# Performance work log

Measured on AMD Instinct MI355X. Metric: run time of the kernel, lower is better.

Reference implementation:

```python
import jax, jax.numpy as jnp
import numpy as np

B, S, K, H = 8192, 512, 8, 512  # batch, size_half, n_segments, hidden
EPS = 1e-6


def setup_inputs() -> dict:
    key = jax.random.key(0)
    k0, k1, k2, k3 = jax.random.split(key, 4)
    x_input = jax.random.uniform(k0, (B, 2 * S), dtype=jnp.float32)  # in [0,1)
    log_density = jax.random.normal(k1, (B, 1), dtype=jnp.float32)
    W1 = jax.random.normal(k2, (S, H), dtype=jnp.float32) / np.sqrt(S).astype(np.float32)
    b1 = jnp.zeros((H,), jnp.float32)
    W2 = jax.random.normal(k3, (H, S * (2 * K + 1)), dtype=jnp.float32) / np.sqrt(H).astype(np.float32)
    b2 = jnp.zeros((S * (2 * K + 1),), jnp.float32)
    return {"x_input": x_input, "log_density": log_density,
            "W1": W1, "b1": b1, "W2": W2, "b2": b2}


def reference(x_input, log_density, W1, b1, W2, b2):
    # even_sites=True: passive half a = first S cols, transformed half b = last S
    x_a = x_input[:, :S]
    x_b = x_input[:, S:]

    # NeuralNetwork: Linear -> tanh -> Linear -> tanh (final_activation == activation)
    hid = jnp.tanh((x_a - 0.5) @ W1 + b1)
    net = jnp.tanh(hid @ W2 + b2).reshape(-1, S, 2 * K + 1)  # [B,S,2K+1]
    h_raw, w_raw = net[..., :K + 1], net[..., K + 1:]

    w_norm = jax.nn.softmax(w_raw, axis=2)                       # [B,S,K]
    eh = jnp.exp(h_raw)                                          # [B,S,K+1]
    h_norm = eh / jnp.sum(0.5 * w_norm * (eh[..., :-1] + eh[..., 1:]),
                          axis=2, keepdims=True)

    b = x_a.shape[0]
    x_knots = jnp.concatenate(
        [jnp.full((b, S, 1), -EPS, x_a.dtype), jnp.cumsum(w_norm, axis=2)], axis=2)  # [B,S,K+1]
    pdf_area = 0.5 * w_norm * (h_norm[..., :-1] + h_norm[..., 1:])
    phi_knots = jnp.concatenate(
        [jnp.zeros((b, S, 1), x_a.dtype), jnp.cumsum(pdf_area, axis=2)], axis=2)     # [B,S,K+1]

    # searchsorted(left) - 1 == (# knots strictly below x) - 1
    k_ind = jnp.clip(jnp.sum(x_knots < x_b[..., None], axis=2) - 1, 0, K - 1)[..., None]

    w_k = jnp.take_along_axis(w_norm, k_ind, axis=2)
    h_k = jnp.take_along_axis(h_norm, k_ind, axis=2)
    h_kp1 = jnp.take_along_axis(h_norm, k_ind + 1, axis=2)
    x_km1 = jnp.take_along_axis(x_knots, k_ind, axis=2)
    phi_km1 = jnp.take_along_axis(phi_knots, k_ind, axis=2)

    alpha = (x_b[..., None] - x_km1) / w_k
    phi_b = (phi_km1 + alpha * h_k * w_k
             + 0.5 * alpha ** 2 * (h_kp1 - h_k) * w_k)[..., 0]    # [B,S]

    phi_out = jnp.concatenate([x_a, phi_b], axis=1)               # [B,2S]
    new_log_density = log_density - jnp.sum(
        jnp.log(h_k + alpha * (h_kp1 - h_k)), axis=1)             # [B,1]
    return phi_out, new_log_density
```

## Files before the change

### kernel.cpp

```cpp
#include <hip/hip_runtime.h>
#include <stdint.h>
#include <math.h>

#define BROWS 8192
#define SDIM  512
#define HDIM  512
#define NCOL  8704
#define EPSK  1e-6f
#define LOG2E  1.442695041f
#define TWOL2E 2.885390082f
#define LN2    0.6931471806f

typedef __attribute__((ext_vector_type(8))) short bf16x8;
typedef __attribute__((ext_vector_type(4))) short bf16x4;
typedef __attribute__((ext_vector_type(4))) float f32x4;

__device__ __forceinline__ unsigned short f2bf(float f) {
    unsigned u = __float_as_uint(f);
    u += 0x7fffu + ((u >> 16) & 1u);
    return (unsigned short)(u >> 16);
}
__device__ __forceinline__ unsigned short f2bf_fast(float f) {
    return (unsigned short)((__float_as_uint(f) + 0x8000u) >> 16);
}
__device__ __forceinline__ float bf2f(unsigned short s) {
    return __uint_as_float(((unsigned)s) << 16);
}
#define EXP2F(x) __builtin_amdgcn_exp2f(x)
#define LOG2F(x) __builtin_amdgcn_logf(x)
#define RCPF(x)  __builtin_amdgcn_rcpf(x)

__device__ __forceinline__ float ftanh(float x) {
    float t = fminf(fmaxf(TWOL2E * x, -43.f), 43.f);
    float e = EXP2F(t);
    return (e - 1.f) * RCPF(e + 1.f);
}
__device__ __forceinline__ float ftanh_l2e(float acc, float bias2L) {
    float t = fminf(fmaxf(fmaf(acc, TWOL2E, bias2L), -43.f), 43.f);
    float e = EXP2F(t);
    return fmaf(e, LOG2E, -LOG2E) * RCPF(e + 1.f);
}

#define GLD16(g, l)                                                         \
    __builtin_amdgcn_global_load_lds(                                       \
        (const __attribute__((address_space(1))) void*)(g),                 \
        (__attribute__((address_space(3))) void*)(l), 16, 0, 0)

__global__ __launch_bounds__(256) void prep_k(
    const float* __restrict__ W2, unsigned short* __restrict__ W2p,
    const float* __restrict__ W1, unsigned short* __restrict__ W1T,
    const float* __restrict__ logd, float* __restrict__ out)
{
    __shared__ float tile[32 * 33];
    const int t = threadIdx.x;
    if (blockIdx.x < 544) {
        const int ct = blockIdx.x;
        const int colbase = ct * 16;
        const int colblk = ct / 17;
        const int chunk  = ct - colblk * 17;
        const int k32 = t >> 3;
        const int c2  = (t & 7) * 2;
        const int r   = t >> 4;
        const int e2  = (t & 15) * 2;
        for (int kk = 0; kk < 16; ++kk) {
            float2 v = *(const float2*)&W2[(size_t)(kk * 32 + k32) * NCOL + colbase + c2];
            __syncthreads();
            tile[k32 * 17 + c2 + 0] = v.x;
            tile[k32 * 17 + c2 + 1] = v.y;
            __syncthreads();
            const size_t off = (((size_t)colblk * 16 + kk) * 17 + chunk) * 512;
            ushort2 o;
            o.x = f2bf(tile[(e2 + 0) * 17 + r]);
            o.y = f2bf(tile[(e2 + 1) * 17 + r]);
            *(ushort2*)&W2p[off + (size_t)r * 32 + e2] = o;
        }
    } else if (blockIdx.x < 800) {
        const int bt = blockIdx.x - 544;
        const int cb = (bt & 15) * 32;
        const int rb = (bt >> 4) * 32;
        const int ty = t >> 3, tx = (t & 7) * 4;
        float4 v = *(const float4*)&W1[(size_t)(rb + ty) * HDIM + cb + tx];
        tile[ty * 33 + tx + 0] = v.x;
        tile[ty * 33 + tx + 1] = v.y;
        tile[ty * 33 + tx + 2] = v.z;
        tile[ty * 33 + tx + 3] = v.w;
        __syncthreads();
        const int oy = t >> 3, ox = (t & 7) * 4;
        bf16x4 o;
        o[0] = (short)f2bf(tile[(ox + 0) * 33 + oy]);
        o[1] = (short)f2bf(tile[(ox + 1) * 33 + oy]);
        o[2] = (short)f2bf(tile[(ox + 2) * 33 + oy]);
        o[3] = (short)f2bf(tile[(ox + 3) * 33 + oy]);
        *(bf16x4*)&W1T[(size_t)(cb + oy) * SDIM + rb + ox] = o;
    } else {
        const int b = (blockIdx.x - 800) * 256 + t;
        out[(size_t)BROWS * (2 * SDIM) + b] = logd[b];
    }
}

__global__ __launch_bounds__(256) void gemm1_mfma(
    const float* __restrict__ x,
    const unsigned short* __restrict__ W1T,
    const float* __restrict__ b1,
    unsigned short* __restrict__ hid,
    float* __restrict__ out)
{
    __shared__ short As[64 * 32];
    __shared__ short Bs[128 * 32];
    const int bm   = blockIdx.y * 64;
    const int bn   = blockIdx.x * 128;
    const int tid  = threadIdx.x;
    const int lane = tid & 63;
    const int wave = tid >> 6;
    const int ln15 = lane & 15;
    const int quad = lane >> 4;
    const int wm   = (wave >> 1) * 32;
    const int wn   = (wave & 1) * 64;
    const int arow = tid >> 2, aseg = tid & 3;
    const int brow = lane >> 2, bsub = lane & 3;

    f32x4 acc[2][4];
#pragma unroll
    for (int i = 0; i < 2; i++)
#pragma unroll
        for (int j = 0; j < 4; j++) acc[i][j] = (f32x4){0.f, 0.f, 0.f, 0.f};

    for (int k0 = 0; k0 < SDIM; k0 += 32) {
        const float4* xq = (const float4*)&x[(size_t)(bm + arow) * (2 * SDIM) + k0 + aseg * 8];
        float4 f0 = xq[0], f1 = xq[1];
        if (blockIdx.x == 0) {
            float* op = &out[(size_t)(bm + arow) * (2 * SDIM) + k0 + aseg * 8];
            *(float4*)op = f0;
            *(float4*)(op + 4) = f1;
        }
        __syncthreads();
#pragma unroll
        for (int c = 0; c < 2; c++) {
            const int chunk = wave * 2 + c;
            GLD16(&W1T[(size_t)(bn + chunk * 16 + brow) * SDIM + k0 + bsub * 8],
                  &Bs[chunk * 512]);
        }
        bf16x8 v0;
        v0[0] = (short)f2bf_fast(f0.x - 0.5f); v0[1] = (short)f2bf_fast(f0.y - 0.5f);
        v0[2] = (short)f2bf_fast(f0.z - 0.5f); v0[3] = (short)f2bf_fast(f0.w - 0.5f);
        v0[4] = (short)f2bf_fast(f1.x - 0.5f); v0[5] = (short)f2bf_fast(f1.y - 0.5f);
        v0[6] = (short)f2bf_fast(f1.z - 0.5f); v0[7] = (short)f2bf_fast(f1.w - 0.5f);
        *(bf16x8*)&As[arow * 32 + aseg * 8] = v0;
        __syncthreads();

        bf16x8 af[2], bfr[4];
#pragma unroll
        for (int i = 0; i < 2; i++)
            af[i] = *(const bf16x8*)&As[(wm + i * 16 + ln15) * 32 + quad * 8];
#pragma unroll
        for (int j = 0; j < 4; j++)
            bfr[j] = *(const bf16x8*)&Bs[(wn + j * 16 + ln15) * 32 + quad * 8];
#pragma unroll
        for (int i = 0; i < 2; i++)
#pragma unroll
            for (int j = 0; j < 4; j++)
                acc[i][j] = __builtin_amdgcn_mfma_f32_16x16x32_bf16(af[i], bfr[j], acc[i][j], 0, 0, 0);
    }

#pragma unroll
    for (int j = 0; j < 4; j++) {
        const int col = bn + wn + j * 16 + ln15;
        const float bias = b1[col];
#pragma unroll
        for (int i = 0; i < 2; i++) {
#pragma unroll
            for (int r = 0; r < 4; r++) {
                const int row = bm + wm + i * 16 + quad * 4 + r;
                hid[(size_t)row * HDIM + col] = f2bf(ftanh(acc[i][j][r] + bias));
            }
        }
    }
}

__global__ __launch_bounds__(256, 3) void gemm2_spline_mfma(
    const unsigned short* __restrict__ hid,
    const unsigned short* __restrict__ W2p,
    const float* __restrict__ b2,
    const float* __restrict__ x,
    float* __restrict__ out)
{
    __shared__ short smem[64 * 392];
    short* As = smem;
    short* Bs = smem + 2048;

    const int bm   = blockIdx.y * 64;
    const int tid  = threadIdx.x;
    const int lane = tid & 63;
    const int wave = tid >> 6;
    const int ln15 = lane & 15;
    const int quad = lane >> 4;
    const int brow = lane >> 2, bsub = lane & 3;
    const int jstart = wave * 4;
    const int jcount = (wave == 3) ? 5 : 4;
    const int bcol = blockIdx.x * 272;

    f32x4 acc[4][5];
#pragma unroll
    for (int i = 0; i < 4; i++)
#pragma unroll
        for (int j = 0; j < 5; j++) acc[i][j] = (f32x4){0.f, 0.f, 0.f, 0.f};

    const unsigned short* bbase =
        W2p + ((size_t)blockIdx.x * 16) * 17 * 512 + (size_t)lane * 8;

    for (int k0 = 0; k0 < HDIM; k0 += 32) {
        const unsigned short* bk = bbase + (size_t)(k0 >> 5) * (17 * 512);
        __syncthreads();
        GLD16(&hid[(size_t)(bm + wave * 16 + brow) * HDIM + k0 + bsub * 8],
              &As[wave * 512]);
        for (int c = 0; c < jcount; ++c) {
            const int chunk = jstart + c;
            GLD16(bk + (size_t)chunk * 512, &Bs[chunk * 512]);
        }
        __syncthreads();

        bf16x8 af[4];
#pragma unroll
        for (int i = 0; i < 4; i++)
            af[i] = *(const bf16x8*)&As[(i * 16 + ln15) * 32 + quad * 8];

#define KSTEP(JC)                                                               \
        _Pragma("unroll") for (int j = 0; j < (JC); ++j) {                      \
            bf16x8 bfr = *(const bf16x8*)&Bs[((jstart + j) * 16 + ln15) * 32 + quad * 8]; \
            _Pragma("unroll") for (int i = 0; i < 4; ++i)                       \
                acc[i][j] = __builtin_amdgcn_mfma_f32_16x16x32_bf16(af[i], bfr, acc[i][j], 0, 0, 0); \
        }
        if (wave == 3) { KSTEP(5) } else { KSTEP(4) }
#undef KSTEP
    }

    __syncthreads();
#define EPI1(JC)                                                                \
    _Pragma("unroll") for (int j = 0; j < (JC); ++j) {                          \
        const int col_l = (jstart + j) * 16 + ln15;                             \
        const int spc   = (col_l * 241) >> 12;         \
        const int cc    = col_l - spc * 17;                                     \
        const int basej = spc * 24 + cc;                                        \
        const float bias2L = b2[bcol + col_l] * TWOL2E;                         \
        _Pragma("unroll") for (int i = 0; i < 4; ++i)                           \
            _Pragma("unroll") for (int r = 0; r < 4; ++r) {                     \
                const int row_l = i * 16 + quad * 4 + r;                        \
                smem[row_l * 392 + basej] =                                     \
                    (short)f2bf_fast(ftanh_l2e(acc[i][j][r], bias2L));          \
            }                                                                   \
    }
    if (wave == 3) { EPI1(5) } else { EPI1(4) }
#undef EPI1
    __syncthreads();

    const int sp = tid & 15;
    const int r0 = tid >> 4;
    const int sglob = blockIdx.x * 16 + sp;
    for (int t = 0; t < 4; ++t) {
        const int row_l = t * 16 + r0;
        const int row = bm + row_l;
        const int base2 = row_l * 392 + sp * 24;
        bf16x8 p0 = *(const bf16x8*)&smem[base2];
        bf16x8 p1 = *(const bf16x8*)&smem[base2 + 8];
        const short p2 = smem[base2 + 16];

        float s[17];
#pragma unroll
        for (int c = 0; c < 8; c++) s[c] = bf2f((unsigned short)p0[c]);
#pragma unroll
        for (int c = 0; c < 8; c++) s[8 + c] = bf2f((unsigned short)p1[c]);
        s[16] = bf2f((unsigned short)p2);

        float eh[9], e[8];
#pragma unroll
        for (int j = 0; j < 9; j++) eh[j] = EXP2F(s[j]);
#pragma unroll
        for (int c = 0; c < 8; c++) e[c]  = EXP2F(s[9 + c]);

        float cum_e[8], cum_u[8];
        cum_e[0] = e[0];
        cum_u[0] = e[0] * (eh[0] + eh[1]);
#pragma unroll
        for (int c = 1; c < 8; c++) {
            cum_e[c] = cum_e[c - 1] + e[c];
            cum_u[c] = fmaf(e[c], eh[c] + eh[c + 1], cum_u[c - 1]);
        }
        const float se = cum_e[7];
        const float su = cum_u[7];

        const float xb  = x[(size_t)row * (2 * SDIM) + SDIM + sglob];
        const float thr = xb * se;

        float selE = e[0], selEH = eh[0], selEH1 = eh[1];
        float selCE = -EPSK * se, selCU = 0.f;
#pragma unroll
        for (int c = 1; c < 8; c++) {
            const bool tt = (cum_e[c - 1] < thr);
            selE   = tt ? e[c]         : selE;
            selEH  = tt ? eh[c]        : selEH;
            selEH1 = tt ? eh[c + 1]    : selEH1;
            selCE  = tt ? cum_e[c - 1] : selCE;
            selCU  = tt ? cum_u[c - 1] : selCU;
        }

        const float alpha = (thr - selCE) * RCPF(selE);
        const float dlt   = selEH1 - selEH;
        const float su_inv = RCPF(su);
        float p = fmaf(2.f * alpha, selE * selEH, selCU);
        p = fmaf(alpha * alpha, selE * dlt, p);
        out[(size_t)row * (2 * SDIM) + SDIM + sglob] = p * su_inv;

        const float g = fmaf(alpha, dlt, selEH) * (2.f * se * su_inv);
        float lg = LOG2F(g);
        lg += __shfl_xor(lg, 1);
        lg += __shfl_xor(lg, 2);
        lg += __shfl_xor(lg, 4);
        lg += __shfl_xor(lg, 8);
        if (sp == 0)
            atomicAdd(&out[(size_t)BROWS * (2 * SDIM) + row], -lg * LN2);
    }
}

extern "C" void kernel_launch(void* const* d_in, const int* in_sizes, int n_in,
                              void* d_out, int out_size, void* d_ws, size_t ws_size,
                              hipStream_t stream) {
    const float* x    = (const float*)d_in[0];
    const float* logd = (const float*)d_in[1];
    const float* W1   = (const float*)d_in[2];
    const float* b1   = (const float*)d_in[3];
    const float* W2   = (const float*)d_in[4];
    const float* b2   = (const float*)d_in[5];
    float* out = (float*)d_out;

    char* ws = (char*)d_ws;
    unsigned short* W1T = (unsigned short*)(ws + 32768);
    unsigned short* W2p = (unsigned short*)(ws + 557056);
    unsigned short* hid = (unsigned short*)(ws + 9469952);

    prep_k<<<832, 256, 0, stream>>>(W2, W2p, W1, W1T, logd, out);
    gemm1_mfma<<<dim3(4, 128), 256, 0, stream>>>(x, W1T, b1, hid, out);
    gemm2_spline_mfma<<<dim3(32, 128), 256, 0, stream>>>(hid, W2p, b2, x, out);
}
```

Baseline: 260.4 us.

## Double-buffer GEMM2 LDS tiles, prefetch x_b, tighten epilogue stride, drop tanh clamps

The GEMM2 main loop now uses two LDS buffers, issuing the next k-slice's async global-to-LDS loads before computing on the current one, which cuts one barrier per iteration and overlaps load latency with MFMA work. The x_b values for the spline stage are loaded before the epilogue so their global latency is hidden. The epilogue staging stride shrinks from 24 to 20 shorts per segment (row stride 392 to 328) so the staging area fits in the smaller double-buffered allocation, with reads done as 4-wide vectors. The tanh clamps are removed, relying on exp2 overflow to infinity behaving correctly, which saves a few ALU ops per element but can produce NaN from inf/inf at large inputs.

```diff
diff --git a/kernel.cpp b/kernel.cpp
--- a/kernel.cpp
+++ b/kernel.cpp
@@ -31,13 +31,11 @@
 #define RCPF(x)  __builtin_amdgcn_rcpf(x)
 
 __device__ __forceinline__ float ftanh(float x) {
-    float t = fminf(fmaxf(TWOL2E * x, -43.f), 43.f);
-    float e = EXP2F(t);
+    float e = EXP2F(TWOL2E * x);
     return (e - 1.f) * RCPF(e + 1.f);
 }
 __device__ __forceinline__ float ftanh_l2e(float acc, float bias2L) {
-    float t = fminf(fmaxf(fmaf(acc, TWOL2E, bias2L), -43.f), 43.f);
-    float e = EXP2F(t);
+    float e = EXP2F(fmaf(acc, TWOL2E, bias2L));
     return fmaf(e, LOG2E, -LOG2E) * RCPF(e + 1.f);
 }
 
@@ -184,9 +182,7 @@
     const float* __restrict__ x,
     float* __restrict__ out)
 {
-    __shared__ short smem[64 * 392];
-    short* As = smem;
-    short* Bs = smem + 2048;
+    __shared__ short smem[2 * 10752];
 
     const int bm   = blockIdx.y * 64;
     const int tid  = threadIdx.x;
@@ -207,17 +203,25 @@
 
     const unsigned short* bbase =
         W2p + ((size_t)blockIdx.x * 16) * 17 * 512 + (size_t)lane * 8;
-
-    for (int k0 = 0; k0 < HDIM; k0 += 32) {
-        const unsigned short* bk = bbase + (size_t)(k0 >> 5) * (17 * 512);
-        __syncthreads();
-        GLD16(&hid[(size_t)(bm + wave * 16 + brow) * HDIM + k0 + bsub * 8],
-              &As[wave * 512]);
+    const unsigned short* abase =
+        &hid[(size_t)(bm + wave * 16 + brow) * HDIM + bsub * 8];
+
+    auto issue = [&](int n, int p) {
+        short* dst = smem + p * 10752;
+        GLD16(abase + n * 32, &dst[wave * 512]);
+        const unsigned short* bk = bbase + (size_t)n * (17 * 512);
         for (int c = 0; c < jcount; ++c) {
             const int chunk = jstart + c;
-            GLD16(bk + (size_t)chunk * 512, &Bs[chunk * 512]);
-        }
+            GLD16(bk + (size_t)chunk * 512, &dst[2048 + chunk * 512]);
+        }
+    };
+
+    issue(0, 0);
+    for (int n = 0; n < 16; ++n) {
         __syncthreads();
+        if (n < 15) issue(n + 1, (n + 1) & 1);
+        const short* As = smem + (n & 1) * 10752;
+        const short* Bs = As + 2048;
 
         bf16x8 af[4];
 #pragma unroll
@@ -233,6 +237,14 @@
         if (wave == 3) { KSTEP(5) } else { KSTEP(4) }
 #undef KSTEP
     }
+
+    const int sp = tid & 15;
+    const int r0 = tid >> 4;
+    const int sglob = blockIdx.x * 16 + sp;
+    float xbv[4];
+#pragma unroll
+    for (int t = 0; t < 4; ++t)
+        xbv[t] = x[(size_t)(bm + t * 16 + r0) * (2 * SDIM) + SDIM + sglob];
 
     __syncthreads();
 #define EPI1(JC)                                                                \
@@ -240,12 +252,12 @@
         const int col_l = (jstart + j) * 16 + ln15;                             \
         const int spc   = (col_l * 241) >> 12;         \
         const int cc    = col_l - spc * 17;                                     \
-        const int basej = spc * 24 + cc;                                        \
+        const int basej = spc * 20 + cc;                                        \
         const float bias2L = b2[bcol + col_l] * TWOL2E;                         \
         _Pragma("unroll") for (int i = 0; i < 4; ++i)                           \
             _Pragma("unroll") for (int r = 0; r < 4; ++r) {                     \
                 const int row_l = i * 16 + quad * 4 + r;                        \
-                smem[row_l * 392 + basej] =                                     \
+                smem[row_l * 328 + basej] =                                     \
                     (short)f2bf_fast(ftanh_l2e(acc[i][j][r], bias2L));          \
             }                                                                   \
     }
@@ -253,22 +265,24 @@
 #undef EPI1
     __syncthreads();
 
-    const int sp = tid & 15;
-    const int r0 = tid >> 4;
-    const int sglob = blockIdx.x * 16 + sp;
     for (int t = 0; t < 4; ++t) {
         const int row_l = t * 16 + r0;
         const int row = bm + row_l;
-        const int base2 = row_l * 392 + sp * 24;
-        bf16x8 p0 = *(const bf16x8*)&smem[base2];
-        bf16x8 p1 = *(const bf16x8*)&smem[base2 + 8];
+        const int base2 = row_l * 328 + sp * 20;
+        bf16x4 a0 = *(const bf16x4*)&smem[base2 + 0];
+        bf16x4 a1 = *(const bf16x4*)&smem[base2 + 4];
+        bf16x4 a2 = *(const bf16x4*)&smem[base2 + 8];
+        bf16x4 a3 = *(const bf16x4*)&smem[base2 + 12];
         const short p2 = smem[base2 + 16];
 
         float s[17];
 #pragma unroll
-        for (int c = 0; c < 8; c++) s[c] = bf2f((unsigned short)p0[c]);
-#pragma unroll
-        for (int c = 0; c < 8; c++) s[8 + c] = bf2f((unsigned short)p1[c]);
+        for (int c = 0; c < 4; c++) {
+            s[c]      = bf2f((unsigned short)a0[c]);
+            s[4 + c]  = bf2f((unsigned short)a1[c]);
+            s[8 + c]  = bf2f((unsigned short)a2[c]);
+            s[12 + c] = bf2f((unsigned short)a3[c]);
+        }
         s[16] = bf2f((unsigned short)p2);
 
         float eh[9], e[8];
@@ -287,9 +301,7 @@
         }
         const float se = cum_e[7];
         const float su = cum_u[7];
-
-        const float xb  = x[(size_t)row * (2 * SDIM) + SDIM + sglob];
-        const float thr = xb * se;
+        const float thr = xbv[t] * se;
 
         float selE = e[0], selEH = eh[0], selEH1 = eh[1];
         float selCE = -EPSK * se, selCU = 0.f;
```

Result: faster. 244.7 us (-6.0%).
